# Performance work log

Measured on AMD Instinct MI355X. Metric: run time of the kernel, lower is better.

Reference implementation:

```python
import jax, jax.numpy as jnp
import numpy as np

NY, NX = 4096, 4096
VP = 3.1415 / 6.0  # particle volume, d=1
DX = 1.0
DY = 1.0


def setup_inputs() -> dict:
    key = jax.random.key(0)
    k1, k2, k3, k4, k5, k6, k7 = jax.random.split(key, 7)
    shape = (1, 1, NY, NX)
    # Eulerian node coordinates (meshgrid)
    xs = jnp.arange(NX, dtype=jnp.float32)
    ys = jnp.arange(NY, dtype=jnp.float32)
    x_grid = jnp.broadcast_to(xs[None, None, None, :], shape)
    y_grid = jnp.broadcast_to(ys[None, None, :, None], shape)
    # Lagrangian particle positions: node coordinate + sub-cell offset
    xp_grid = x_grid + jax.random.uniform(k1, shape, jnp.float32, -0.5, 0.5)
    yp_grid = y_grid + jax.random.uniform(k2, shape, jnp.float32, -0.5, 0.5)
    vx_grid = jax.random.normal(k3, shape, jnp.float32)
    vy_grid = jax.random.normal(k4, shape, jnp.float32)
    Fx_grid = jax.random.normal(k5, shape, jnp.float32)
    Fy_grid = jax.random.normal(k6, shape, jnp.float32)
    mask = (jax.random.uniform(k7, shape, jnp.float32) < 0.3).astype(jnp.float32)
    return {"xp_grid": xp_grid, "yp_grid": yp_grid, "x_grid": x_grid,
            "y_grid": y_grid, "vx_grid": vx_grid, "vy_grid": vy_grid,
            "Fx_grid": Fx_grid, "Fy_grid": Fy_grid, "mask": mask}


def reference(xp_grid, yp_grid, x_grid, y_grid, vx_grid, vy_grid, Fx_grid, Fy_grid, mask):
    # coupling_backward: interpolate particle quantities to Eulerian nodes
    # via a 3x3 linear-spline stencil of torch.roll-shifted fields.
    dt = xp_grid.dtype
    zero = jnp.zeros_like(xp_grid)
    alpha = zero
    alpha_u = zero
    alpha_v = zero
    Fx = zero
    Fy = zero
    inv_area = 1.0 / (DX * DY)
    for i in range(3):
        for j in range(3):
            sh = (j - 1, i - 1)
            sgn_x = jnp.roll(xp_grid, sh, axis=(2, 3)) - x_grid
            sgn_y = jnp.roll(yp_grid, sh, axis=(2, 3)) - y_grid
            Sx = jnp.where(sgn_x >= 0, jnp.float32(1.0), jnp.float32(-1.0)).astype(dt)
            Sy = jnp.where(sgn_y >= 0, jnp.float32(1.0), jnp.float32(-1.0)).astype(dt)
            xii = (2.0 * sgn_x - Sx * DX) / DX
            phi = (2.0 * sgn_y - Sy * DY) / DY
            in_x = ((xii >= -1.0) & (xii <= 1.0)).astype(dt)
            in_y = ((phi >= -1.0) & (phi <= 1.0)).astype(dt)
            N_xii = 0.5 * (1.0 - Sx * xii) * in_x
            N_phi = 0.5 * (1.0 - Sy * phi) * in_y
            w = N_xii * N_phi * mask * VP * inv_area  # per-tap spline weight
            alpha = alpha + w
            alpha_u = alpha_u + w * jnp.roll(vx_grid, sh, axis=(2, 3))
            alpha_v = alpha_v + w * jnp.roll(vy_grid, sh, axis=(2, 3))
            Fx = Fx + w * jnp.roll(Fx_grid, sh, axis=(2, 3))
            Fy = Fy + w * jnp.roll(Fy_grid, sh, axis=(2, 3))
    return jnp.stack([alpha, alpha_u, alpha_v, Fx, Fy])
```

## Files before the change

### kernel.cpp

```cpp
#include <hip/hip_runtime.h>


typedef float v4f __attribute__((ext_vector_type(4)));

static constexpr int NXd = 4096;
static constexpr int NYd = 4096;

__device__ __forceinline__ void load_window(const float* __restrict__ row,
                                            int x0, int xl, int xr, float w[6]) {
    v4f v = *reinterpret_cast<const v4f*>(row + x0);
    w[0] = row[xl];
    w[1] = v[0]; w[2] = v[1]; w[3] = v[2]; w[4] = v[3];
    w[5] = row[xr];
}

__global__ __launch_bounds__(256) void ai4dem_kernel(
    const float* __restrict__ xp, const float* __restrict__ yp,
    const float* __restrict__ vx, const float* __restrict__ vy,
    const float* __restrict__ fxg, const float* __restrict__ fyg,
    const float* __restrict__ mask, float* __restrict__ out)
{
    const int x0 = (blockIdx.x * 256 + threadIdx.x) * 4;
    const int y  = blockIdx.y;

    const int xl = (x0 == 0)         ? (NXd - 1) : (x0 - 1);
    const int xr = (x0 + 4 >= NXd)   ? 0         : (x0 + 4);

    const float yf = (float)y;

    float accA[4] = {0.f, 0.f, 0.f, 0.f};
    float accU[4] = {0.f, 0.f, 0.f, 0.f};
    float accV[4] = {0.f, 0.f, 0.f, 0.f};
    float accX[4] = {0.f, 0.f, 0.f, 0.f};
    float accY[4] = {0.f, 0.f, 0.f, 0.f};

    #pragma unroll
    for (int dy = -1; dy <= 1; ++dy) {
        int yy = y + dy;
        yy = (yy < 0) ? (NYd - 1) : ((yy >= NYd) ? 0 : yy);
        const size_t rb = (size_t)yy * NXd;

        float wxp[6], wyp[6], wvx[6], wvy[6], wfx[6], wfy[6];
        load_window(xp  + rb, x0, xl, xr, wxp);
        load_window(yp  + rb, x0, xl, xr, wyp);
        load_window(vx  + rb, x0, xl, xr, wvx);
        load_window(vy  + rb, x0, xl, xr, wvy);
        load_window(fxg + rb, x0, xl, xr, wfx);
        load_window(fyg + rb, x0, xl, xr, wfy);

        #pragma unroll
        for (int k = 0; k < 4; ++k) {
            const float xf = (float)(x0 + k);
            #pragma unroll
            for (int c = 0; c < 3; ++c) {
                const int wi = k + c;
                float nx = fmaxf(1.0f - fabsf(wxp[wi] - xf), 0.0f);
                float ny = fmaxf(1.0f - fabsf(wyp[wi] - yf), 0.0f);
                float wgt = nx * ny;
                accA[k] += wgt;
                accU[k] = fmaf(wgt, wvx[wi], accU[k]);
                accV[k] = fmaf(wgt, wvy[wi], accV[k]);
                accX[k] = fmaf(wgt, wfx[wi], accX[k]);
                accY[k] = fmaf(wgt, wfy[wi], accY[k]);
            }
        }
    }

    const float VPf = (float)(3.1415 / 6.0);
    const size_t ob    = (size_t)y * NXd + x0;
    const size_t plane = (size_t)NXd * NYd;

    v4f mv = *reinterpret_cast<const v4f*>(mask + ob);
    float m[4] = { mv[0] * VPf, mv[1] * VPf, mv[2] * VPf, mv[3] * VPf };

    v4f o;
    o[0] = accA[0] * m[0]; o[1] = accA[1] * m[1]; o[2] = accA[2] * m[2]; o[3] = accA[3] * m[3];
    __builtin_nontemporal_store(o, reinterpret_cast<v4f*>(out + ob));

    o[0] = accU[0] * m[0]; o[1] = accU[1] * m[1]; o[2] = accU[2] * m[2]; o[3] = accU[3] * m[3];
    __builtin_nontemporal_store(o, reinterpret_cast<v4f*>(out + plane + ob));

    o[0] = accV[0] * m[0]; o[1] = accV[1] * m[1]; o[2] = accV[2] * m[2]; o[3] = accV[3] * m[3];
    __builtin_nontemporal_store(o, reinterpret_cast<v4f*>(out + 2 * plane + ob));

    o[0] = accX[0] * m[0]; o[1] = accX[1] * m[1]; o[2] = accX[2] * m[2]; o[3] = accX[3] * m[3];
    __builtin_nontemporal_store(o, reinterpret_cast<v4f*>(out + 3 * plane + ob));

    o[0] = accY[0] * m[0]; o[1] = accY[1] * m[1]; o[2] = accY[2] * m[2]; o[3] = accY[3] * m[3];
    __builtin_nontemporal_store(o, reinterpret_cast<v4f*>(out + 4 * plane + ob));
}

extern "C" void kernel_launch(void* const* d_in, const int* in_sizes, int n_in,
                              void* d_out, int out_size, void* d_ws, size_t ws_size,
                              hipStream_t stream) {
    const float* xp   = (const float*)d_in[0];
    const float* yp   = (const float*)d_in[1];
    const float* vx   = (const float*)d_in[4];
    const float* vy   = (const float*)d_in[5];
    const float* fxg  = (const float*)d_in[6];
    const float* fyg  = (const float*)d_in[7];
    const float* mask = (const float*)d_in[8];
    float* out = (float*)d_out;

    dim3 block(256, 1, 1);
    dim3 grid(NXd / (256 * 4), NYd, 1);
    hipLaunchKernelGGL(ai4dem_kernel, grid, block, 0, stream,
                       xp, yp, vx, vy, fxg, fyg, mask, out);
}
```

Baseline: 758.3 us.

## Use 2D thread blocks and streamline weight computation with 32-bit offsets

Changes the block shape from 256x1 to 64x4 threads, so each block covers four adjacent rows and vertically neighbouring threads reuse the same input rows through cache. It also computes the y-hat factor once per window element instead of per tap, precomputes all twelve weights, and then loads each field window just before it is used to lower register pressure. Address math moves to 32-bit offsets. Shorter row segments per block may reduce horizontal coalescing width.

Measured after the change: 738.2 us. 1.03x faster.

```diff
diff --git a/kernel.cpp b/kernel.cpp
--- a/kernel.cpp
+++ b/kernel.cpp
@@ -6,12 +6,17 @@
 static constexpr int NXd = 4096;
 static constexpr int NYd = 4096;
 
-__device__ __forceinline__ void load_window(const float* __restrict__ row,
-                                            int x0, int xl, int xr, float w[6]) {
-    v4f v = *reinterpret_cast<const v4f*>(row + x0);
-    w[0] = row[xl];
+__device__ __forceinline__ float hat(float s) {
+    return fmaxf(1.0f - fabsf(s), 0.0f);
+}
+
+__device__ __forceinline__ void load_window6(const float* __restrict__ base,
+                                             int voff, int voffl, int voffr,
+                                             float w[6]) {
+    v4f v = *reinterpret_cast<const v4f*>(base + voff);
+    w[0] = base[voffl];
     w[1] = v[0]; w[2] = v[1]; w[3] = v[2]; w[4] = v[3];
-    w[5] = row[xr];
+    w[5] = base[voffr];
 }
 
 __global__ __launch_bounds__(256) void ai4dem_kernel(
@@ -20,50 +25,77 @@
     const float* __restrict__ fxg, const float* __restrict__ fyg,
     const float* __restrict__ mask, float* __restrict__ out)
 {
-    const int x0 = (blockIdx.x * 256 + threadIdx.x) * 4;
-    const int y  = blockIdx.y;
+    const int tx = threadIdx.x;
+    const int ty = threadIdx.y;
+    const int x0 = (blockIdx.x * 64 + tx) * 4;
+    const int y  = blockIdx.y * 4 + ty;
 
-    const int xl = (x0 == 0)         ? (NXd - 1) : (x0 - 1);
-    const int xr = (x0 + 4 >= NXd)   ? 0         : (x0 + 4);
+    const int xl = (x0 == 0)       ? (NXd - 1) : (x0 - 1);
+    const int xr = (x0 + 4 >= NXd) ? 0         : (x0 + 4);
+    const float yf  = (float)y;
+    const float xf0 = (float)x0;
 
-    const float yf = (float)y;
-
-    float accA[4] = {0.f, 0.f, 0.f, 0.f};
-    float accU[4] = {0.f, 0.f, 0.f, 0.f};
-    float accV[4] = {0.f, 0.f, 0.f, 0.f};
-    float accX[4] = {0.f, 0.f, 0.f, 0.f};
-    float accY[4] = {0.f, 0.f, 0.f, 0.f};
+    float accA[4] = {0.f,0.f,0.f,0.f};
+    float accU[4] = {0.f,0.f,0.f,0.f};
+    float accV[4] = {0.f,0.f,0.f,0.f};
+    float accX[4] = {0.f,0.f,0.f,0.f};
+    float accY[4] = {0.f,0.f,0.f,0.f};
 
     #pragma unroll
     for (int dy = -1; dy <= 1; ++dy) {
         int yy = y + dy;
         yy = (yy < 0) ? (NYd - 1) : ((yy >= NYd) ? 0 : yy);
-        const size_t rb = (size_t)yy * NXd;
+        const int rb    = yy * NXd;
+        const int voff  = rb + x0;
+        const int voffl = rb + xl;
+        const int voffr = rb + xr;
 
-        float wxp[6], wyp[6], wvx[6], wvy[6], wfx[6], wfy[6];
-        load_window(xp  + rb, x0, xl, xr, wxp);
-        load_window(yp  + rb, x0, xl, xr, wyp);
-        load_window(vx  + rb, x0, xl, xr, wvx);
-        load_window(vy  + rb, x0, xl, xr, wvy);
-        load_window(fxg + rb, x0, xl, xr, wfx);
-        load_window(fyg + rb, x0, xl, xr, wfy);
+        float wxp[6], wyp[6];
+        load_window6(xp, voff, voffl, voffr, wxp);
+        load_window6(yp, voff, voffl, voffr, wyp);
 
         #pragma unroll
-        for (int k = 0; k < 4; ++k) {
-            const float xf = (float)(x0 + k);
+        for (int i = 0; i < 6; ++i) wyp[i] = hat(wyp[i] - yf);
+
+        float w[12];
+        #pragma unroll
+        for (int k = 0; k < 4; ++k)
             #pragma unroll
-            for (int c = 0; c < 3; ++c) {
-                const int wi = k + c;
-                float nx = fmaxf(1.0f - fabsf(wxp[wi] - xf), 0.0f);
-                float ny = fmaxf(1.0f - fabsf(wyp[wi] - yf), 0.0f);
-                float wgt = nx * ny;
-                accA[k] += wgt;
-                accU[k] = fmaf(wgt, wvx[wi], accU[k]);
-                accV[k] = fmaf(wgt, wvy[wi], accV[k]);
-                accX[k] = fmaf(wgt, wfx[wi], accX[k]);
-                accY[k] = fmaf(wgt, wfy[wi], accY[k]);
-            }
-        }
+            for (int c = 0; c < 3; ++c)
+                w[k*3 + c] = hat(wxp[k + c] - (xf0 + (float)k)) * wyp[k + c];
+
+        #pragma unroll
+        for (int k = 0; k < 4; ++k)
+            accA[k] += (w[k*3] + w[k*3+1]) + w[k*3+2];
+
+        float win[6];
+        load_window6(vx, voff, voffl, voffr, win);
+        #pragma unroll
+        for (int k = 0; k < 4; ++k)
+            accU[k] = fmaf(w[k*3+2], win[k+2],
+                      fmaf(w[k*3+1], win[k+1],
+                      fmaf(w[k*3+0], win[k+0], accU[k])));
+
+        load_window6(vy, voff, voffl, voffr, win);
+        #pragma unroll
+        for (int k = 0; k < 4; ++k)
+            accV[k] = fmaf(w[k*3+2], win[k+2],
+                      fmaf(w[k*3+1], win[k+1],
+                      fmaf(w[k*3+0], win[k+0], accV[k])));
+
+        load_window6(fxg, voff, voffl, voffr, win);
+        #pragma unroll
+        for (int k = 0; k < 4; ++k)
+            accX[k] = fmaf(w[k*3+2], win[k+2],
+                      fmaf(w[k*3+1], win[k+1],
+                      fmaf(w[k*3+0], win[k+0], accX[k])));
+
+        load_window6(fyg, voff, voffl, voffr, win);
+        #pragma unroll
+        for (int k = 0; k < 4; ++k)
+            accY[k] = fmaf(w[k*3+2], win[k+2],
+                      fmaf(w[k*3+1], win[k+1],
+                      fmaf(w[k*3+0], win[k+0], accY[k])));
     }
 
     const float VPf = (float)(3.1415 / 6.0);
@@ -74,20 +106,20 @@
     float m[4] = { mv[0] * VPf, mv[1] * VPf, mv[2] * VPf, mv[3] * VPf };
 
     v4f o;
-    o[0] = accA[0] * m[0]; o[1] = accA[1] * m[1]; o[2] = accA[2] * m[2]; o[3] = accA[3] * m[3];
+    o[0] = accA[0]*m[0]; o[1] = accA[1]*m[1]; o[2] = accA[2]*m[2]; o[3] = accA[3]*m[3];
     __builtin_nontemporal_store(o, reinterpret_cast<v4f*>(out + ob));
 
-    o[0] = accU[0] * m[0]; o[1] = accU[1] * m[1]; o[2] = accU[2] * m[2]; o[3] = accU[3] * m[3];
+    o[0] = accU[0]*m[0]; o[1] = accU[1]*m[1]; o[2] = accU[2]*m[2]; o[3] = accU[3]*m[3];
     __builtin_nontemporal_store(o, reinterpret_cast<v4f*>(out + plane + ob));
 
-    o[0] = accV[0] * m[0]; o[1] = accV[1] * m[1]; o[2] = accV[2] * m[2]; o[3] = accV[3] * m[3];
-    __builtin_nontemporal_store(o, reinterpret_cast<v4f*>(out + 2 * plane + ob));
+    o[0] = accV[0]*m[0]; o[1] = accV[1]*m[1]; o[2] = accV[2]*m[2]; o[3] = accV[3]*m[3];
+    __builtin_nontemporal_store(o, reinterpret_cast<v4f*>(out + 2*plane + ob));
 
-    o[0] = accX[0] * m[0]; o[1] = accX[1] * m[1]; o[2] = accX[2] * m[2]; o[3] = accX[3] * m[3];
-    __builtin_nontemporal_store(o, reinterpret_cast<v4f*>(out + 3 * plane + ob));
+    o[0] = accX[0]*m[0]; o[1] = accX[1]*m[1]; o[2] = accX[2]*m[2]; o[3] = accX[3]*m[3];
+    __builtin_nontemporal_store(o, reinterpret_cast<v4f*>(out + 3*plane + ob));
 
-    o[0] = accY[0] * m[0]; o[1] = accY[1] * m[1]; o[2] = accY[2] * m[2]; o[3] = accY[3] * m[3];
-    __builtin_nontemporal_store(o, reinterpret_cast<v4f*>(out + 4 * plane + ob));
+    o[0] = accY[0]*m[0]; o[1] = accY[1]*m[1]; o[2] = accY[2]*m[2]; o[3] = accY[3]*m[3];
+    __builtin_nontemporal_store(o, reinterpret_cast<v4f*>(out + 4*plane + ob));
 }
 
 extern "C" void kernel_launch(void* const* d_in, const int* in_sizes, int n_in,
@@ -102,8 +134,8 @@
     const float* mask = (const float*)d_in[8];
     float* out = (float*)d_out;
 
-    dim3 block(256, 1, 1);
-    dim3 grid(NXd / (256 * 4), NYd, 1);
+    dim3 block(64, 4, 1);
+    dim3 grid(NXd / 256, NYd / 4, 1);
     hipLaunchKernelGGL(ai4dem_kernel, grid, block, 0, stream,
                        xp, yp, vx, vy, fxg, fyg, mask, out);
 }
```
